# Optimization experiments

Hardware: AMD Instinct MI355X
Metric: run time of the kernel (lower is better)

Reference implementation:

```python
import jax, jax.numpy as jnp
import numpy as np

MARGIN = 0.3


def setup_inputs() -> dict:
    key = jax.random.key(0)
    k1, k2 = jax.random.split(key)
    inputs = jax.random.normal(k1, (8192, 128), dtype=jnp.float32)
    targets = jax.random.randint(k2, (8192,), 0, 512, dtype=jnp.int64)
    return {"inputs": inputs, "targets": targets}


def reference(inputs, targets):
    # inputs: [n, d], targets: [n]
    sq = jnp.sum(inputs * inputs, axis=1)  # [n]
    # dist[i,j] = ||x_i||^2 + ||x_j||^2 - 2 x_i . x_j
    dist = sq[:, None] + sq[None, :] - 2.0 * (inputs @ inputs.T)
    dist = jnp.sqrt(jnp.clip(dist, 1e-12, None))  # [n, n]
    mask = targets[:, None] == targets[None, :]  # True where same label
    # batch-hard mining: hardest positive (max) and hardest negative (min) per row.
    # Diagonal is always True, so every row has at least one positive.
    dist_ap = jnp.max(jnp.where(mask, dist, -jnp.inf), axis=1)  # [n]
    dist_an = jnp.min(jnp.where(mask, jnp.inf, dist), axis=1)  # [n]
    # MarginRankingLoss with y=1: mean(max(0, margin - (dist_an - dist_ap)))
    loss = jnp.mean(jnp.maximum(0.0, MARGIN - (dist_an - dist_ap)))
    prec = jnp.mean((dist_an > dist_ap).astype(jnp.float32))
    return loss, prec
```

## Files before the change

kernel.cpp:

```cpp
#include <hip/hip_runtime.h>
#include <hip/hip_bf16.h>
#include <math.h>

#define N 8192
#define D 128
#define MARGIN 0.3f

#define NSTRIP 64
#define BPS 8
#define GRID_MAIN (NSTRIP * BPS)
#define NWIN 66

typedef float f32x4 __attribute__((ext_vector_type(4)));
typedef short bf16x8 __attribute__((ext_vector_type(8)));
typedef unsigned short u16x8 __attribute__((ext_vector_type(8)));

#define AS1 __attribute__((address_space(1)))
#define AS3 __attribute__((address_space(3)))

__device__ inline void gload_lds16(const void* g, void* l) {
    __builtin_amdgcn_global_load_lds((AS1 void*)(void*)(g), (AS3 void*)(l), 16, 0, 0);
}

__device__ inline unsigned short f2bf(float f) {
    unsigned u = __float_as_uint(f);
    unsigned r = (u + 0x7FFFu + ((u >> 16) & 1u)) >> 16;
    return (unsigned short)r;
}

__global__ __launch_bounds__(256) void convert_kernel(const float* __restrict__ X,
                                                      unsigned short* __restrict__ Xb,
                                                      float* __restrict__ sq,
                                                      unsigned* __restrict__ ap2,
                                                      unsigned* __restrict__ an2) {
    int tid = threadIdx.x;
    int row = blockIdx.x * 16 + (tid >> 4);
    int l = tid & 15;
    const float4* p = reinterpret_cast<const float4*>(X + (size_t)row * D + l * 8);
    float4 u = p[0];
    float4 v = p[1];
    float s = u.x*u.x + u.y*u.y + u.z*u.z + u.w*u.w
            + v.x*v.x + v.y*v.y + v.z*v.z + v.w*v.w;
    u16x8 o;
    o[0] = f2bf(u.x); o[1] = f2bf(u.y); o[2] = f2bf(u.z); o[3] = f2bf(u.w);
    o[4] = f2bf(v.x); o[5] = f2bf(v.y); o[6] = f2bf(v.z); o[7] = f2bf(v.w);
    *reinterpret_cast<u16x8*>(Xb + (size_t)row * D + l * 8) = o;
    #pragma unroll
    for (int off = 8; off >= 1; off >>= 1) s += __shfl_xor(s, off);
    if (l == 0) {
        sq[row] = s;
        ap2[row] = 0u;
        an2[row] = 0x7F7F7F7Fu;
    }
}

__global__ __launch_bounds__(256, 2) void triplet_main(
        const unsigned short* __restrict__ Xb,
        const int* __restrict__ lbl,
        const float* __restrict__ sq,
        unsigned* __restrict__ ap2,
        unsigned* __restrict__ an2) {
    __shared__ unsigned short As[128 * D];
    __shared__ unsigned short Bs[2][64 * D];

    const int bi = blockIdx.x >> 3;
    const int s  = blockIdx.x & 7;
    const int base = s * 8 + (s < 2 ? s : 2);
    const int cnt  = (s < 2) ? 9 : 8;
    const int jwin0 = 2 * bi;

    const int tid = threadIdx.x;
    const int w = tid >> 6;
    const int lane = tid & 63;
    const int wr = w >> 1;
    const int wc = w & 1;
    const int quad = lane >> 4;
    const int lx = lane & 15;
    const int i0 = bi * 128;

    int lbl_i[16];
    float sqi_r[16];
    #pragma unroll
    for (int tr = 0; tr < 4; ++tr)
        #pragma unroll
        for (int v = 0; v < 4; ++v) {
            int row = i0 + wr * 64 + tr * 16 + quad * 4 + v;
            lbl_i[tr * 4 + v] = lbl[row];
            sqi_r[tr * 4 + v] = sq[row];
        }

    float m_ap[16], m_an[16];
    #pragma unroll
    for (int q = 0; q < 16; ++q) { m_ap[q] = -INFINITY; m_an[q] = INFINITY; }

    #pragma unroll
    for (int t = 0; t < 8; ++t) {
        int rbase = w * 32 + t * 4;
        int r = rbase + quad;
        int gc = lx ^ (r & 7);
        gload_lds16(Xb + (size_t)(i0 + r) * D + gc * 8, &As[rbase * D]);
    }
    {
        int jj0 = (jwin0 + base) & 127;
        #pragma unroll
        for (int t = 0; t < 4; ++t) {
            int rbase = w * 16 + t * 4;
            int r = rbase + quad;
            int gc = lx ^ (r & 7);
            gload_lds16(Xb + (size_t)(jj0 * 64 + r) * D + gc * 8, &Bs[0][rbase * D]);
        }
    }
    __syncthreads();

    bf16x8 af[4][4];
    #pragma unroll
    for (int ks = 0; ks < 4; ++ks)
        #pragma unroll
        for (int tr = 0; tr < 4; ++tr) {
            int rA = wr * 64 + tr * 16 + lx;
            int sc = (ks * 4 + quad) ^ (lx & 7);
            af[ks][tr] = *reinterpret_cast<const bf16x8*>(&As[rA * D + sc * 8]);
        }

    #pragma unroll 1
    for (int t = 0; t < cnt; ++t) {
        const int o = base + t;
        const int jj = (jwin0 + o) & 127;
        const int cb = t & 1;

        if (t + 1 < cnt) {
            int jjn = (jwin0 + o + 1) & 127;
            #pragma unroll
            for (int tt = 0; tt < 4; ++tt) {
                int rbase = w * 16 + tt * 4;
                int r = rbase + quad;
                int gc = lx ^ (r & 7);
                gload_lds16(Xb + (size_t)(jjn * 64 + r) * D + gc * 8,
                            &Bs[1 - cb][rbase * D]);
            }
        }
        float sqj[2]; int lblj[2];
        #pragma unroll
        for (int tc = 0; tc < 2; ++tc) {
            int jc = jj * 64 + wc * 32 + tc * 16 + lx;
            sqj[tc] = sq[jc];
            lblj[tc] = lbl[jc];
        }

        f32x4 acc[4][2];
        #pragma unroll
        for (int a = 0; a < 4; ++a)
            #pragma unroll
            for (int c = 0; c < 2; ++c)
                acc[a][c] = (f32x4){0.f, 0.f, 0.f, 0.f};

        #pragma unroll
        for (int ks = 0; ks < 4; ++ks) {
            bf16x8 bf[2];
            #pragma unroll
            for (int tc = 0; tc < 2; ++tc) {
                int rB = wc * 32 + tc * 16 + lx;
                int sc = (ks * 4 + quad) ^ (lx & 7);
                bf[tc] = *reinterpret_cast<const bf16x8*>(&Bs[cb][rB * D + sc * 8]);
            }
            #pragma unroll
            for (int tr = 0; tr < 4; ++tr)
                #pragma unroll
                for (int tc = 0; tc < 2; ++tc)
                    acc[tr][tc] = __builtin_amdgcn_mfma_f32_16x16x32_bf16(
                        af[ks][tr], bf[tc], acc[tr][tc], 0, 0, 0);
        }

        __syncthreads();

        const bool jmine = (o >= 2) & (o < 64);
        #pragma unroll
        for (int tc = 0; tc < 2; ++tc) {
            float mApJ = -INFINITY, mAnJ = INFINITY;
            #pragma unroll
            for (int tr = 0; tr < 4; ++tr) {
                #pragma unroll
                for (int v = 0; v < 4; ++v) {
                    int q = tr * 4 + v;
                    float dot2 = -2.f * acc[tr][tc][v];
                    float vi = sqj[tc] + dot2;
                    float vj = sqi_r[q] + dot2;
                    bool same = (lblj[tc] == lbl_i[q]);
                    m_ap[q] = same ? fmaxf(m_ap[q], vi) : m_ap[q];
                    m_an[q] = same ? m_an[q] : fminf(m_an[q], vi);
                    mApJ = same ? fmaxf(mApJ, vj) : mApJ;
                    mAnJ = same ? mAnJ : fminf(mAnJ, vj);
                }
            }
            if (jmine) {
                #pragma unroll
                for (int off = 16; off <= 32; off <<= 1) {
                    mApJ = fmaxf(mApJ, __shfl_xor(mApJ, off));
                    mAnJ = fminf(mAnJ, __shfl_xor(mAnJ, off));
                }
                if (quad == 0) {
                    int jc = jj * 64 + wc * 32 + tc * 16 + lx;
                    float vap = fmaxf(sqj[tc] + mApJ, 1e-12f);
                    float van = fmaxf(sqj[tc] + mAnJ, 1e-12f);
                    atomicMax(&ap2[jc], __float_as_uint(vap));
                    atomicMin(&an2[jc], __float_as_uint(van));
                }
            }
        }
    }

    #pragma unroll
    for (int off = 8; off >= 1; off >>= 1) {
        #pragma unroll
        for (int q = 0; q < 16; ++q) {
            m_ap[q] = fmaxf(m_ap[q], __shfl_xor(m_ap[q], off));
            m_an[q] = fminf(m_an[q], __shfl_xor(m_an[q], off));
        }
    }
    if (lx == 0) {
        #pragma unroll
        for (int tr = 0; tr < 4; ++tr) {
            #pragma unroll
            for (int v = 0; v < 4; ++v) {
                int q = tr * 4 + v;
                int row = i0 + wr * 64 + tr * 16 + quad * 4 + v;
                float vap = fmaxf(sqi_r[q] + m_ap[q], 1e-12f);
                float van = fmaxf(sqi_r[q] + m_an[q], 1e-12f);
                atomicMax(&ap2[row], __float_as_uint(vap));
                atomicMin(&an2[row], __float_as_uint(van));
            }
        }
    }
}

__global__ __launch_bounds__(1024) void finalize_kernel(const unsigned* __restrict__ ap2,
                                                        const unsigned* __restrict__ an2,
                                                        float* __restrict__ out) {
    int tid = threadIdx.x;
    float ls = 0.f, ps = 0.f;
    for (int row = tid; row < N; row += 1024) {
        float ap = sqrtf(__uint_as_float(ap2[row]));
        float an = sqrtf(__uint_as_float(an2[row]));
        ls += fmaxf(0.f, MARGIN - (an - ap));
        ps += (an > ap) ? 1.f : 0.f;
    }
    #pragma unroll
    for (int off = 32; off >= 1; off >>= 1) {
        ls += __shfl_xor(ls, off);
        ps += __shfl_xor(ps, off);
    }
    __shared__ float red[2][16];
    int w = tid >> 6;
    if ((tid & 63) == 0) { red[0][w] = ls; red[1][w] = ps; }
    __syncthreads();
    if (tid == 0) {
        float L = 0.f, P = 0.f;
        #pragma unroll
        for (int i = 0; i < 16; ++i) { L += red[0][i]; P += red[1][i]; }
        out[0] = L / (float)N;
        out[1] = P / (float)N;
    }
}

extern "C" void kernel_launch(void* const* d_in, const int* in_sizes, int n_in,
                              void* d_out, int out_size, void* d_ws, size_t ws_size,
                              hipStream_t stream) {
    const float* X = (const float*)d_in[0];
    const int* lbl = (const int*)d_in[1];
    float* out = (float*)d_out;

    float* sq = (float*)d_ws;
    unsigned* ap2 = (unsigned*)d_ws + N;
    unsigned* an2 = (unsigned*)d_ws + 2 * N;
    unsigned short* Xb = (unsigned short*)((char*)d_ws + 3 * N * sizeof(unsigned));

    convert_kernel<<<N / 16, 256, 0, stream>>>(X, Xb, sq, ap2, an2);
    triplet_main<<<GRID_MAIN, 256, 0, stream>>>(Xb, lbl, sq, ap2, an2);
    finalize_kernel<<<1, 1024, 0, stream>>>(ap2, an2, out);
}
```

Baseline: 97.39 us.

## Single-buffer B tile, reload A fragments, raise occupancy to three blocks

Drops the double-buffered B tile to one LDS buffer and reloads A fragments from LDS each k-step instead of holding them in registers. This cuts LDS and register pressure so three blocks can fit per CU. Work is re-split into 11 blocks per strip of 6 column tiles each, replacing the uneven 8/9 split. The next B tile is now prefetched only during the epilogue, which costs an extra barrier per tile and more LDS reads in exchange for higher occupancy and more blocks in flight.

```diff
diff --git a/kernel.cpp b/kernel.cpp
--- a/kernel.cpp
+++ b/kernel.cpp
@@ -7,9 +7,9 @@
 #define MARGIN 0.3f
 
 #define NSTRIP 64
-#define BPS 8
+#define BPS 11
+#define TPB 6
 #define GRID_MAIN (NSTRIP * BPS)
-#define NWIN 66
 
 typedef float f32x4 __attribute__((ext_vector_type(4)));
 typedef short bf16x8 __attribute__((ext_vector_type(8)));
@@ -54,19 +54,18 @@
     }
 }
 
-__global__ __launch_bounds__(256, 2) void triplet_main(
+__global__ __launch_bounds__(256, 3) void triplet_main(
         const unsigned short* __restrict__ Xb,
         const int* __restrict__ lbl,
         const float* __restrict__ sq,
         unsigned* __restrict__ ap2,
         unsigned* __restrict__ an2) {
     __shared__ unsigned short As[128 * D];
-    __shared__ unsigned short Bs[2][64 * D];
-
-    const int bi = blockIdx.x >> 3;
-    const int s  = blockIdx.x & 7;
-    const int base = s * 8 + (s < 2 ? s : 2);
-    const int cnt  = (s < 2) ? 9 : 8;
+    __shared__ unsigned short Bs[64 * D];
+
+    const int bi = blockIdx.x / BPS;
+    const int s  = blockIdx.x - bi * BPS;
+    const int base = s * TPB;
     const int jwin0 = 2 * bi;
 
     const int tid = threadIdx.x;
@@ -107,71 +106,66 @@
             int rbase = w * 16 + t * 4;
             int r = rbase + quad;
             int gc = lx ^ (r & 7);
-            gload_lds16(Xb + (size_t)(jj0 * 64 + r) * D + gc * 8, &Bs[0][rbase * D]);
+            gload_lds16(Xb + (size_t)(jj0 * 64 + r) * D + gc * 8, &Bs[rbase * D]);
         }
     }
     __syncthreads();
 
-    bf16x8 af[4][4];
-    #pragma unroll
-    for (int ks = 0; ks < 4; ++ks)
-        #pragma unroll
-        for (int tr = 0; tr < 4; ++tr) {
-            int rA = wr * 64 + tr * 16 + lx;
-            int sc = (ks * 4 + quad) ^ (lx & 7);
-            af[ks][tr] = *reinterpret_cast<const bf16x8*>(&As[rA * D + sc * 8]);
-        }
-
     #pragma unroll 1
-    for (int t = 0; t < cnt; ++t) {
+    for (int t = 0; t < TPB; ++t) {
         const int o = base + t;
         const int jj = (jwin0 + o) & 127;
-        const int cb = t & 1;
-
-        if (t + 1 < cnt) {
+
+        float sqj[2]; int lblj[2];
+        #pragma unroll
+        for (int tc = 0; tc < 2; ++tc) {
+            int jc = jj * 64 + wc * 32 + tc * 16 + lx;
+            sqj[tc] = sq[jc];
+            lblj[tc] = lbl[jc];
+        }
+
+        f32x4 acc[4][2];
+        #pragma unroll
+        for (int a = 0; a < 4; ++a)
+            #pragma unroll
+            for (int c = 0; c < 2; ++c)
+                acc[a][c] = (f32x4){0.f, 0.f, 0.f, 0.f};
+
+        #pragma unroll
+        for (int ks = 0; ks < 4; ++ks) {
+            bf16x8 af[4], bf[2];
+            #pragma unroll
+            for (int tr = 0; tr < 4; ++tr) {
+                int rA = wr * 64 + tr * 16 + lx;
+                int sc = (ks * 4 + quad) ^ (lx & 7);
+                af[tr] = *reinterpret_cast<const bf16x8*>(&As[rA * D + sc * 8]);
+            }
+            #pragma unroll
+            for (int tc = 0; tc < 2; ++tc) {
+                int rB = wc * 32 + tc * 16 + lx;
+                int sc = (ks * 4 + quad) ^ (lx & 7);
+                bf[tc] = *reinterpret_cast<const bf16x8*>(&Bs[rB * D + sc * 8]);
+            }
+            #pragma unroll
+            for (int tr = 0; tr < 4; ++tr)
+                #pragma unroll
+                for (int tc = 0; tc < 2; ++tc)
+                    acc[tr][tc] = __builtin_amdgcn_mfma_f32_16x16x32_bf16(
+                        af[tr], bf[tc], acc[tr][tc], 0, 0, 0);
+        }
+
+        __syncthreads();
+
+        if (t + 1 < TPB) {
             int jjn = (jwin0 + o + 1) & 127;
             #pragma unroll
             for (int tt = 0; tt < 4; ++tt) {
                 int rbase = w * 16 + tt * 4;
                 int r = rbase + quad;
                 int gc = lx ^ (r & 7);
-                gload_lds16(Xb + (size_t)(jjn * 64 + r) * D + gc * 8,
-                            &Bs[1 - cb][rbase * D]);
-            }
-        }
-        float sqj[2]; int lblj[2];
-        #pragma unroll
-        for (int tc = 0; tc < 2; ++tc) {
-            int jc = jj * 64 + wc * 32 + tc * 16 + lx;
-            sqj[tc] = sq[jc];
-            lblj[tc] = lbl[jc];
-        }
-
-        f32x4 acc[4][2];
-        #pragma unroll
-        for (int a = 0; a < 4; ++a)
-            #pragma unroll
-            for (int c = 0; c < 2; ++c)
-                acc[a][c] = (f32x4){0.f, 0.f, 0.f, 0.f};
-
-        #pragma unroll
-        for (int ks = 0; ks < 4; ++ks) {
-            bf16x8 bf[2];
-            #pragma unroll
-            for (int tc = 0; tc < 2; ++tc) {
-                int rB = wc * 32 + tc * 16 + lx;
-                int sc = (ks * 4 + quad) ^ (lx & 7);
-                bf[tc] = *reinterpret_cast<const bf16x8*>(&Bs[cb][rB * D + sc * 8]);
-            }
-            #pragma unroll
-            for (int tr = 0; tr < 4; ++tr)
-                #pragma unroll
-                for (int tc = 0; tc < 2; ++tc)
-                    acc[tr][tc] = __builtin_amdgcn_mfma_f32_16x16x32_bf16(
-                        af[ks][tr], bf[tc], acc[tr][tc], 0, 0, 0);
-        }
-
-        __syncthreads();
+                gload_lds16(Xb + (size_t)(jjn * 64 + r) * D + gc * 8, &Bs[rbase * D]);
+            }
+        }
 
         const bool jmine = (o >= 2) & (o < 64);
         #pragma unroll
@@ -207,6 +201,8 @@
                 }
             }
         }
+
+        if (t + 1 < TPB) __syncthreads();
     }
 
     #pragma unroll
```

Result: faster. 93.40 us (-4.1%).
